# Kernel tuning notes

Measured on AMD Instinct MI355X. Metric: run time of the kernel, lower is better.

Reference implementation:

```python
import jax, jax.numpy as jnp
import numpy as np

HID, NH, HD = 1024, 16, 64
WIN = 512
DFF, NE, TOPK = 4096, 8, 2
B, S = 1, 2048
EPS = 1e-6


def _rope_rotation_matrix(seq_len, head_dim):
    # Block-diagonal 2x2 rotation matrices per position (standard RoPE as a fused matrix).
    pos = np.arange(seq_len, dtype=np.float64)
    inv_freq = 1.0 / (10000.0 ** (np.arange(0, head_dim, 2, dtype=np.float64) / head_dim))
    ang = pos[:, None] * inv_freq[None, :]            # [S, HD/2]
    c, s = np.cos(ang), np.sin(ang)
    R = np.zeros((seq_len, head_dim, head_dim), np.float32)
    i = np.arange(0, head_dim, 2)
    R[:, i, i] = c
    R[:, i + 1, i + 1] = c
    R[:, i, i + 1] = -s
    R[:, i + 1, i] = s
    return jnp.asarray(R)


def setup_inputs() -> dict:
    key = jax.random.key(0)
    ks = jax.random.split(key, 10)
    init = lambda k, shape, scale=0.02: (jax.random.normal(k, shape, jnp.float32) * scale)
    return {
        "x": jax.random.normal(ks[0], (B, S, HID), jnp.float32),
        "rotation_matrix": _rope_rotation_matrix(S, HD),
        "rms1_w": jnp.ones((HID,), jnp.float32),
        "wq": init(ks[1], (HID, HID)),
        "wk": init(ks[2], (HID, HID)),
        "wv": init(ks[3], (HID, HID)),
        "wo": init(ks[4], (HID, HID)),
        "rms2_w": jnp.ones((HID,), jnp.float32),
        "gate_w": init(ks[5], (HID, NE)),
        "w1": init(ks[6], (NE, HID, DFF)),
        "w2": init(ks[7], (NE, DFF, HID)),
        "w3": init(ks[8], (NE, HID, DFF)),
    }


def _rmsnorm(x, w):
    return x * jax.lax.rsqrt(jnp.mean(x * x, axis=-1, keepdims=True) + EPS) * w


def reference(x, rotation_matrix, rms1_w, wq, wk, wv, wo, rms2_w, gate_w, w1, w2, w3):
    b, s, _ = x.shape
    # --- sliding-window attention with fused RoPE rotation matrix ---
    y = _rmsnorm(x, rms1_w)
    q = (y @ wq).reshape(b, s, NH, HD).transpose(0, 2, 1, 3)  # bhsd
    k = (y @ wk).reshape(b, s, NH, HD).transpose(0, 2, 1, 3)
    v = (y @ wv).reshape(b, s, NH, HD).transpose(0, 2, 1, 3)
    q = jnp.einsum('bhsd,sde->bhse', q, rotation_matrix)
    k = jnp.einsum('bhsd,sde->bhse', k, rotation_matrix)
    scores = jnp.einsum('bhqd,bhkd->bhqk', q, k) / np.float32(np.sqrt(HD))
    idx = jnp.arange(s)
    mask = (idx[:, None] >= idx[None, :]) & (idx[:, None] - idx[None, :] < WIN)
    scores = jnp.where(mask[None, None], scores, jnp.float32(-1e9))
    att = jax.nn.softmax(scores, axis=-1)
    attn_out = jnp.einsum('bhqk,bhkd->bhqd', att, v)
    attn_out = attn_out.transpose(0, 2, 1, 3).reshape(b, s, HID) @ wo
    x = x + attn_out
    # --- MoE SwiGLU FFN with top-k routing ---
    y = _rmsnorm(x, rms2_w)
    t = y.reshape(b * s, HID)                                  # [T, D]
    logits = t @ gate_w                                        # [T, E]
    top_v, top_i = jax.lax.top_k(logits, TOPK)
    gates = jax.nn.softmax(top_v, axis=-1)                     # [T, K]
    w_full = jnp.zeros((b * s, NE), t.dtype).at[
        jnp.arange(b * s)[:, None], top_i].set(gates)          # [T, E] sparse routing weights
    h = jax.nn.silu(jnp.einsum('td,edf->etf', t, w1)) * jnp.einsum('td,edf->etf', t, w3)
    expert_out = jnp.einsum('etf,efd->etd', h, w2)             # [E, T, D]
    moe = jnp.einsum('te,etd->td', w_full, expert_out).reshape(b, s, HID)
    return x + moe
```

## Files before the change

### kernel.cpp

```cpp
#include <hip/hip_runtime.h>
#include <hip/hip_bf16.h>
#include <stdint.h>


#define S_ 2048
#define HID_ 1024
#define NH_ 16
#define HD_ 64
#define WIN_ 512
#define DFF_ 4096
#define NE_ 8

typedef unsigned short u16;
typedef __attribute__((ext_vector_type(8))) short short8;
typedef __attribute__((ext_vector_type(4))) float f32x4;

__device__ __forceinline__ u16 f2bf(float f) {
  union { float f; unsigned u; } v; v.f = f;
  unsigned r = (v.u + 0x7FFFu + ((v.u >> 16) & 1u)) >> 16;
  return (u16)r;
}
__device__ __forceinline__ float bf2f(u16 b) {
  union { unsigned u; float f; } v; v.u = ((unsigned)b) << 16;
  return v.f;
}

__device__ __forceinline__ void gload16(const void* g, void* l) {
  __builtin_amdgcn_global_load_lds(
      (const __attribute__((address_space(1))) void*)g,
      (__attribute__((address_space(3))) void*)l, 16, 0, 0);
}

template <int N>
__device__ __forceinline__ void waitcnt_vm() {
  static_assert(N == 0 || N == 4 || N == 8 || N == 12 || N == 16 || N == 24,
                "unsupported vmcnt");
  if constexpr (N == 0) asm volatile("s_waitcnt vmcnt(0)" ::: "memory");
  else if constexpr (N == 4) asm volatile("s_waitcnt vmcnt(4)" ::: "memory");
  else if constexpr (N == 8) asm volatile("s_waitcnt vmcnt(8)" ::: "memory");
  else if constexpr (N == 12) asm volatile("s_waitcnt vmcnt(12)" ::: "memory");
  else if constexpr (N == 16) asm volatile("s_waitcnt vmcnt(16)" ::: "memory");
  else if constexpr (N == 24) asm volatile("s_waitcnt vmcnt(24)" ::: "memory");
}

__global__ __launch_bounds__(256) void convT_f32_k(const float* __restrict__ W,
                                                   u16* __restrict__ WT,
                                                   int K, int N, size_t matStride) {
  __shared__ u16 t[64][72];
  const float* Wm = W + (size_t)blockIdx.z * matStride;
  u16* WTm = WT + (size_t)blockIdx.z * matStride;
  int n0 = blockIdx.x * 64, k0 = blockIdx.y * 64;
  int tid = threadIdx.x;
  int cw = (tid & 15) * 4, rr = tid >> 4;
#pragma unroll
  for (int p = 0; p < 4; ++p) {
    int r = p * 16 + rr;
    float4 v = *(const float4*)&Wm[(size_t)(k0 + r) * N + n0 + cw];
    t[cw][r] = f2bf(v.x);
    t[cw + 1][r] = f2bf(v.y);
    t[cw + 2][r] = f2bf(v.z);
    t[cw + 3][r] = f2bf(v.w);
  }
  __syncthreads();
#pragma unroll
  for (int p = 0; p < 4; ++p) {
    int n = p * 16 + rr;
    ushort4 pk = *(const ushort4*)&t[n][cw];
    *(ushort4*)&WTm[(size_t)(n0 + n) * K + k0 + cw] = pk;
  }
}

__global__ __launch_bounds__(256) void convT_qkvo_k(const float* __restrict__ wq,
                                                    const float* __restrict__ wk,
                                                    const float* __restrict__ wv,
                                                    const float* __restrict__ wo,
                                                    u16* __restrict__ outT) {
  __shared__ u16 t[64][72];
  int z = blockIdx.z;
  const float* Wm = (z == 0) ? wq : (z == 1) ? wk : (z == 2) ? wv : wo;
  u16* WTm = outT + (size_t)z * HID_ * HID_;
  int n0 = blockIdx.x * 64, k0 = blockIdx.y * 64;
  int tid = threadIdx.x;
  int cw = (tid & 15) * 4, rr = tid >> 4;
#pragma unroll
  for (int p = 0; p < 4; ++p) {
    int r = p * 16 + rr;
    float4 v = *(const float4*)&Wm[(size_t)(k0 + r) * HID_ + n0 + cw];
    t[cw][r] = f2bf(v.x);
    t[cw + 1][r] = f2bf(v.y);
    t[cw + 2][r] = f2bf(v.z);
    t[cw + 3][r] = f2bf(v.w);
  }
  __syncthreads();
#pragma unroll
  for (int p = 0; p < 4; ++p) {
    int n = p * 16 + rr;
    ushort4 pk = *(const ushort4*)&t[n][cw];
    *(ushort4*)&WTm[(size_t)(n0 + n) * HID_ + k0 + cw] = pk;
  }
}

__global__ __launch_bounds__(256) void convT_u16_k(const u16* __restrict__ W,
                                                   u16* __restrict__ WT,
                                                   int K, int N, size_t matStride) {
  __shared__ u16 t[64][66];
  const u16* Wm = W + (size_t)blockIdx.z * matStride;
  u16* WTm = WT + (size_t)blockIdx.z * matStride;
  int n0 = blockIdx.x * 64, k0 = blockIdx.y * 64;
  int tid = threadIdx.x;
  int c2 = (tid & 31) * 2, rr = tid >> 5;
#pragma unroll
  for (int it = 0; it < 8; ++it) {
    int r = it * 8 + rr;
    unsigned vv = *(const unsigned*)&Wm[(size_t)(k0 + r) * N + n0 + c2];
    t[c2][r] = (u16)vv;
    t[c2 + 1][r] = (u16)(vv >> 16);
  }
  __syncthreads();
#pragma unroll
  for (int it = 0; it < 8; ++it) {
    int n = it * 8 + rr;
    unsigned pk = (unsigned)t[n][c2] | ((unsigned)t[n][c2 + 1] << 16);
    *(unsigned*)&WTm[(size_t)(n0 + n) * K + k0 + c2] = pk;
  }
}

__global__ __launch_bounds__(256) void rope_tab_k(const float* __restrict__ rot,
                                                  float* __restrict__ cost,
                                                  float* __restrict__ sint) {
  int id = blockIdx.x * 256 + threadIdx.x;
  if (id >= S_ * 32) return;
  int s = id >> 5, j = id & 31;
  cost[id] = rot[(size_t)s * 4096 + (size_t)(2 * j) * 64 + 2 * j];
  sint[id] = rot[(size_t)s * 4096 + (size_t)(2 * j + 1) * 64 + 2 * j];
}

__global__ __launch_bounds__(256) void rms1_k(const float* __restrict__ x,
                                              const float* __restrict__ rw,
                                              u16* __restrict__ y) {
  int row = blockIdx.x, tid = threadIdx.x;
  const float4 v = *(const float4*)&x[(size_t)row * HID_ + tid * 4];
  float ss = v.x * v.x + v.y * v.y + v.z * v.z + v.w * v.w;
#pragma unroll
  for (int o = 32; o; o >>= 1) ss += __shfl_xor(ss, o);
  __shared__ float red[4];
  if ((tid & 63) == 0) red[tid >> 6] = ss;
  __syncthreads();
  float rstd = rsqrtf((red[0] + red[1] + red[2] + red[3]) * (1.f / HID_) + 1e-6f);
  const float4 w4 = *(const float4*)&rw[tid * 4];
  ushort4 o4;
  o4.x = f2bf(v.x * rstd * w4.x);
  o4.y = f2bf(v.y * rstd * w4.y);
  o4.z = f2bf(v.z * rstd * w4.z);
  o4.w = f2bf(v.w * rstd * w4.w);
  *(ushort4*)&y[(size_t)row * HID_ + tid * 4] = o4;
}

__global__ __launch_bounds__(256) void rms2_gate_k(const float* __restrict__ x2,
                                                   const float* __restrict__ rw,
                                                   const float* __restrict__ gw,
                                                   u16* __restrict__ y2,
                                                   float* __restrict__ logits) {
  int row = blockIdx.x, tid = threadIdx.x;
  int wv = tid >> 6, ln = tid & 63;
  const float4 v = *(const float4*)&x2[(size_t)row * HID_ + tid * 4];
  float ss = v.x * v.x + v.y * v.y + v.z * v.z + v.w * v.w;
#pragma unroll
  for (int o = 32; o; o >>= 1) ss += __shfl_xor(ss, o);
  __shared__ float red[4];
  __shared__ float lred[4][8];
  if (ln == 0) red[wv] = ss;
  __syncthreads();
  float rstd = rsqrtf((red[0] + red[1] + red[2] + red[3]) * (1.f / HID_) + 1e-6f);
  const float4 w4 = *(const float4*)&rw[tid * 4];
  float yv[4];
  yv[0] = v.x * rstd * w4.x; yv[1] = v.y * rstd * w4.y;
  yv[2] = v.z * rstd * w4.z; yv[3] = v.w * rstd * w4.w;
  ushort4 o4;
  o4.x = f2bf(yv[0]); o4.y = f2bf(yv[1]); o4.z = f2bf(yv[2]); o4.w = f2bf(yv[3]);
  *(ushort4*)&y2[(size_t)row * HID_ + tid * 4] = o4;
  float le[8] = {0, 0, 0, 0, 0, 0, 0, 0};
  int d0 = tid * 4;
#pragma unroll
  for (int j = 0; j < 4; ++j) {
    const float* grow = &gw[(size_t)(d0 + j) * NE_];
#pragma unroll
    for (int e = 0; e < 8; ++e) le[e] += yv[j] * grow[e];
  }
#pragma unroll
  for (int e = 0; e < 8; ++e) {
    float t = le[e];
#pragma unroll
    for (int o = 32; o; o >>= 1) t += __shfl_xor(t, o);
    le[e] = t;
  }
  if (ln == 0)
#pragma unroll
    for (int e = 0; e < 8; ++e) lred[wv][e] = le[e];
  __syncthreads();
  if (tid < 8)
    logits[(size_t)row * NE_ + tid] =
        lred[0][tid] + lred[1][tid] + lred[2][tid] + lred[3][tid];
}

__global__ __launch_bounds__(1024) void route_k(const float* __restrict__ logits,
                                                int* __restrict__ topi,
                                                float* __restrict__ topg,
                                                int* __restrict__ counts,
                                                int* __restrict__ ebase,
                                                int* __restrict__ slot_token,
                                                int* __restrict__ slot_of) {
  __shared__ int cnt[8], bas[8], rnk[8];
  int tid = threadIdx.x;
  if (tid < 8) { cnt[tid] = 0; rnk[tid] = 0; }
  __syncthreads();
  int e0[2], e1[2];
  float g0[2], g1[2];
#pragma unroll
  for (int s = 0; s < 2; ++s) {
    int t = tid * 2 + s;
    const float* lg = &logits[(size_t)t * NE_];
    float v0 = -1e30f; int i0 = 0;
#pragma unroll
    for (int e = 0; e < 8; ++e) {
      float x = lg[e];
      if (x > v0) { v0 = x; i0 = e; }
    }
    float v1 = -1e30f; int i1 = 0;
#pragma unroll
    for (int e = 0; e < 8; ++e) {
      if (e == i0) continue;
      float x = lg[e];
      if (x > v1) { v1 = x; i1 = e; }
    }
    float ex = __expf(v1 - v0);
    e0[s] = i0; e1[s] = i1;
    g0[s] = 1.f / (1.f + ex);
    g1[s] = ex / (1.f + ex);
    topi[t * 2] = i0; topi[t * 2 + 1] = i1;
    topg[t * 2] = g0[s]; topg[t * 2 + 1] = g1[s];
    atomicAdd(&cnt[i0], 1);
    atomicAdd(&cnt[i1], 1);
  }
  __syncthreads();
  if (tid == 0) {
    int s = 0;
    for (int e = 0; e < 8; ++e) { bas[e] = s; s += cnt[e]; }
  }
  __syncthreads();
#pragma unroll
  for (int s = 0; s < 2; ++s) {
    int t = tid * 2 + s;
    int p0 = bas[e0[s]] + atomicAdd(&rnk[e0[s]], 1);
    int p1 = bas[e1[s]] + atomicAdd(&rnk[e1[s]], 1);
    slot_token[p0] = t; slot_token[p1] = t;
    slot_of[t * 2] = p0; slot_of[t * 2 + 1] = p1;
  }
  if (tid < 8) { counts[tid] = cnt[tid]; ebase[tid] = bas[tid]; }
}

template <int MODE, int SLOTS>
__global__ __launch_bounds__(256, (SLOTS <= 3 ? 3 : (SLOTS <= 5 ? 2 : 1)))
void gemm3_k(
    const u16* __restrict__ A, const u16* __restrict__ B0,
    const u16* __restrict__ B1, const u16* __restrict__ B2, int K,
    const int* __restrict__ ecnt, const int* __restrict__ ebase,
    const float* __restrict__ cost, const float* __restrict__ sint,
    const float* __restrict__ xres, float* __restrict__ outf,
    u16* __restrict__ o0, u16* __restrict__ o1, u16* __restrict__ o2) {
  constexpr int WVM = 4 * (SLOTS - 2);
  __shared__ alignas(16) char smem[SLOTS * 16384];

  int n0 = blockIdx.x * 128, m0 = blockIdx.y * 128;
  int cnt = 0, base = 0, kc = 0;
  const u16* Bp;
  u16* outb = o0;
  float* pout = outf;
  int rope = 0;
  if constexpr (MODE == 0) {
    int z = blockIdx.z;
    Bp = (z == 0) ? B0 : (z == 1) ? B1 : B2;
    outb = (z == 0) ? o0 : (z == 1) ? o1 : o2;
    rope = (z < 2) ? 1 : 0;
  } else if constexpr (MODE == 1) {
    Bp = B0;
  } else if constexpr (MODE == 4) {
    int e = blockIdx.z >> 1;
    kc = blockIdx.z & 1;
    cnt = ecnt[e]; base = ebase[e];
    if (m0 >= cnt) return;
    Bp = B0 + (size_t)e * HID_ * DFF_;
    pout = outf + (size_t)kc * ((size_t)2 * S_ * HID_);
  } else {
    int e = blockIdx.z;
    cnt = ecnt[e]; base = ebase[e];
    if (m0 >= cnt) return;
    Bp = B0 + (size_t)e * HID_ * DFF_;
  }

  int tid = threadIdx.x, w = tid >> 6, l = tid & 63, lo = l & 15, g = l >> 4;
  int wm = w >> 1, wn = w & 1;
  int KT = K >> 5;
  size_t rb = (MODE == 4) ? (size_t)DFF_ * 2 : (size_t)K * 2;
  size_t kcoff = (MODE == 4) ? (size_t)kc * (size_t)(DFF_ / 2) * 2 : 0;

  int lrow = l >> 2, lu = l & 3;
  const char* pA[2];
  const char* pB[2];
  int ldOff[2];
#pragma unroll
  for (int j = 0; j < 2; ++j) {
    int rA = j * 64 + w * 16 + lrow;
    int swz = (lu ^ ((rA >> 1) & 3)) << 4;
    size_t arow;
    if constexpr (MODE == 3 || MODE == 4) {
      arow = (size_t)(base + min(m0 + rA, cnt - 1));
    } else {
      arow = (size_t)(m0 + rA);
    }
    pA[j] = (const char*)A + arow * rb + kcoff + swz;
    pB[j] = (const char*)Bp + (size_t)(n0 + rA) * rb + kcoff + swz;
    ldOff[j] = (j * 64 + w * 16) * 64;
  }

  auto stage = [&](int t) {
    char* s = smem + (t % SLOTS) * 16384;
    size_t kb = (size_t)t * 64;
    gload16(pA[0] + kb, s + ldOff[0]);
    gload16(pA[1] + kb, s + ldOff[1]);
    gload16(pB[0] + kb, s + 8192 + ldOff[0]);
    gload16(pB[1] + kb, s + 8192 + ldOff[1]);
  };

  f32x4 acc[4][4];
#pragma unroll
  for (int i = 0; i < 4; ++i)
#pragma unroll
    for (int j = 0; j < 4; ++j) acc[i][j] = (f32x4){0.f, 0.f, 0.f, 0.f};

#pragma unroll
  for (int s = 0; s < SLOTS - 1; ++s) stage(min(s, KT - 1));
  waitcnt_vm<WVM>();
  __builtin_amdgcn_s_barrier();

  for (int t = 0; t < KT; ++t) {
    char* s = smem + (t % SLOTS) * 16384;
    stage(min(t + SLOTS - 1, KT - 1));
    short8 afr[4], bfr[4];
#pragma unroll
    for (int mi = 0; mi < 4; ++mi) {
      int r = wm * 64 + mi * 16 + lo;
      afr[mi] = *(const short8*)(s + r * 64 + ((g ^ ((r >> 1) & 3)) << 4));
    }
#pragma unroll
    for (int ni = 0; ni < 4; ++ni) {
      int r = wn * 64 + ni * 16 + lo;
      bfr[ni] = *(const short8*)(s + 8192 + r * 64 + ((g ^ ((r >> 1) & 3)) << 4));
    }
    asm volatile("s_waitcnt lgkmcnt(0)" ::: "memory");
    __builtin_amdgcn_s_setprio(1);
#pragma unroll
    for (int mi = 0; mi < 4; ++mi)
#pragma unroll
      for (int ni = 0; ni < 4; ++ni)
        acc[mi][ni] = __builtin_amdgcn_mfma_f32_16x16x32_bf16(afr[mi], bfr[ni], acc[mi][ni], 0, 0, 0);
    __builtin_amdgcn_s_setprio(0);
    if (t + 1 < KT)
      waitcnt_vm<WVM>();
    else
      waitcnt_vm<0>();
    __builtin_amdgcn_s_barrier();
  }
  asm volatile("s_waitcnt vmcnt(0) lgkmcnt(0)" ::: "memory");

#pragma unroll
  for (int mi = 0; mi < 4; ++mi) {
    int lr = wm * 64 + mi * 16 + g * 4;
#pragma unroll
    for (int ni = 0; ni < 4; ++ni) {
      int c = n0 + wn * 64 + ni * 16 + lo;
#pragma unroll
      for (int r = 0; r < 4; ++r) {
        float v = acc[mi][ni][r];
        if constexpr (MODE == 0) {
          int row = m0 + lr + r;
          float p = __shfl_xor(v, 1);
          if (rope) {
            int dd = c & 63;
            float co = cost[(size_t)row * 32 + (dd >> 1)];
            float si = sint[(size_t)row * 32 + (dd >> 1)];
            v = (dd & 1) ? (co * v - si * p) : (co * v + si * p);
          }
          outb[((size_t)(c >> 6) * S_ + row) * HD_ + (c & 63)] = f2bf(v);
        } else if constexpr (MODE == 1) {
          int row = m0 + lr + r;
          outf[(size_t)row * HID_ + c] = v + xres[(size_t)row * HID_ + c];
        } else if constexpr (MODE == 4) {
          int m = m0 + lr + r;
          if (m < cnt) pout[(size_t)(base + m) * HID_ + c] = v;
        } else {
          int m = m0 + lr + r;
          if (m < cnt) outb[(size_t)(base + m) * HID_ + c] = f2bf(v);
        }
      }
    }
  }
}

template <int TPB, int MODE>
__global__ __launch_bounds__(TPB, 2) void gemm5_k(
    const u16* __restrict__ A, const u16* __restrict__ B0,
    const u16* __restrict__ B1, int K, const int* __restrict__ ecnt,
    const int* __restrict__ ebase, const int* __restrict__ slot_token,
    u16* __restrict__ o0, u16* __restrict__ o1) {
  constexpr int NW = TPB / 64;
  constexpr int WN = NW / 2;
  constexpr int BM = TPB / 2;
  constexpr int MROW = BM / 2;
  constexpr int MI = MROW / 16;
  constexpr int MH = MI / 2;
  constexpr int ABYTES = BM * 128;
  __shared__ alignas(16) char smem[ABYTES * 4];
  char* ldsA = smem;
  char* ldsB = smem + 2 * ABYTES;

  int n0 = blockIdx.x * BM, m0 = blockIdx.y * BM;
  int cnt = 0, base = 0;
  const u16* Bp;
  u16* outb;
  {
    int e = blockIdx.z >> 1, mat = blockIdx.z & 1;
    cnt = ecnt[e]; base = ebase[e];
    if (m0 >= cnt) return;
    Bp = (mat ? B1 : B0) + (size_t)e * DFF_ * HID_;
    outb = mat ? o1 : o0;
  }

  int tid = threadIdx.x, w = tid >> 6, l = tid & 63, lo = l & 15, g = l >> 4;
  int wm = w / WN, wn = w % WN;
  int KT = K >> 6;
  size_t rb = (size_t)K * 2;

  int lrow = l >> 3, lu = l & 7;
  const char* pA[4];
  const char* pB[4];
  int ldOff[4];
#pragma unroll
  for (int j = 0; j < 4; ++j) {
    int rA = j * (BM / 4) + w * 8 + lrow;
    int swz = (lu ^ (rA & 7)) << 4;
    size_t arow = (size_t)slot_token[base + min(m0 + rA, cnt - 1)];
    pA[j] = (const char*)A + arow * rb + swz;
    pB[j] = (const char*)Bp + (size_t)(n0 + rA) * rb + swz;
    ldOff[j] = (j * (BM / 4) + w * 8) * 128;
  }

  auto stA = [&](int t, int j) {
    gload16(pA[j] + (size_t)t * 128, ldsA + (t & 1) * ABYTES + ldOff[j]);
  };
  auto stB = [&](int t, int j) {
    gload16(pB[j] + (size_t)t * 128, ldsB + (t & 1) * ABYTES + ldOff[j]);
  };
  auto rdA = [&](int d, int mi, int kh) {
    int row = wm * MROW + mi * 16 + lo;
    return *(const short8*)(ldsA + d * ABYTES + row * 128 +
                            (((kh * 4 + g) ^ (row & 7)) << 4));
  };
  auto rdB = [&](int d, int ni, int kh) {
    int row = wn * 64 + ni * 16 + lo;
    return *(const short8*)(ldsB + d * ABYTES + row * 128 +
                            (((kh * 4 + g) ^ (row & 7)) << 4));
  };

  f32x4 acc[MI][4];
#pragma unroll
  for (int i = 0; i < MI; ++i)
#pragma unroll
    for (int j = 0; j < 4; ++j) acc[i][j] = (f32x4){0.f, 0.f, 0.f, 0.f};

  stB(0, 0); stB(0, 1); stB(0, 2); stB(0, 3);
  stA(0, 0); stA(0, 2);
  stA(0, 1); stA(0, 3);
  {
    int t1 = min(1, KT - 1);
    stA(t1, 0); stA(t1, 2);
  }
  asm volatile("s_waitcnt vmcnt(4)" ::: "memory");
  __builtin_amdgcn_s_barrier();

  for (int t = 0; t < KT; ++t) {
    int d = t & 1;
    int tn = min(t + 1, KT - 1);
    int tn2 = min(t + 2, KT - 1);
    short8 afr[MH], bfr[4];
    stB(tn, 0); stB(tn, 1);
#pragma unroll
    for (int i = 0; i < MH; ++i) afr[i] = rdA(d, i, 0);
#pragma unroll
    for (int n = 0; n < 4; ++n) bfr[n] = rdB(d, n, 0);
    asm volatile("s_waitcnt lgkmcnt(0)" ::: "memory");
    __builtin_amdgcn_s_setprio(1);
#pragma unroll
    for (int i = 0; i < MH; ++i)
#pragma unroll
      for (int n = 0; n < 4; ++n)
        acc[i][n] = __builtin_amdgcn_mfma_f32_16x16x32_bf16(afr[i], bfr[n], acc[i][n], 0, 0, 0);
    __builtin_amdgcn_s_setprio(0);
    asm volatile("s_waitcnt vmcnt(4)" ::: "memory");
    __builtin_amdgcn_s_barrier();
    stB(tn, 2); stB(tn, 3);
#pragma unroll
    for (int i = 0; i < MH; ++i) afr[i] = rdA(d, MH + i, 0);
    asm volatile("s_waitcnt lgkmcnt(0)" ::: "memory");
    __builtin_amdgcn_s_setprio(1);
#pragma unroll
    for (int i = 0; i < MH; ++i)
#pragma unroll
      for (int n = 0; n < 4; ++n)
        acc[MH + i][n] = __builtin_amdgcn_mfma_f32_16x16x32_bf16(afr[i], bfr[n], acc[MH + i][n], 0, 0, 0);
    __builtin_amdgcn_s_setprio(0);
    __builtin_amdgcn_s_barrier();
    stA(tn, 1); stA(tn, 3);
#pragma unroll
    for (int i = 0; i < MH; ++i) afr[i] = rdA(d, i, 1);
#pragma unroll
    for (int n = 0; n < 4; ++n) bfr[n] = rdB(d, n, 1);
    asm volatile("s_waitcnt lgkmcnt(0)" ::: "memory");
    __builtin_amdgcn_s_setprio(1);
#pragma unroll
    for (int i = 0; i < MH; ++i)
#pragma unroll
      for (int n = 0; n < 4; ++n)
        acc[i][n] = __builtin_amdgcn_mfma_f32_16x16x32_bf16(afr[i], bfr[n], acc[i][n], 0, 0, 0);
    __builtin_amdgcn_s_setprio(0);
    __builtin_amdgcn_s_barrier();
    stA(tn2, 0); stA(tn2, 2);
#pragma unroll
    for (int i = 0; i < MH; ++i) afr[i] = rdA(d, MH + i, 1);
    asm volatile("s_waitcnt lgkmcnt(0)" ::: "memory");
    __builtin_amdgcn_s_setprio(1);
#pragma unroll
    for (int i = 0; i < MH; ++i)
#pragma unroll
      for (int n = 0; n < 4; ++n)
        acc[MH + i][n] = __builtin_amdgcn_mfma_f32_16x16x32_bf16(afr[i], bfr[n], acc[MH + i][n], 0, 0, 0);
    __builtin_amdgcn_s_setprio(0);
    asm volatile("s_waitcnt vmcnt(4)" ::: "memory");
    __builtin_amdgcn_s_barrier();
  }
  asm volatile("s_waitcnt vmcnt(0) lgkmcnt(0)" ::: "memory");

#pragma unroll
  for (int mi = 0; mi < MI; ++mi) {
    int lr = wm * MROW + mi * 16 + g * 4;
#pragma unroll
    for (int ni = 0; ni < 4; ++ni) {
      int c = n0 + wn * 64 + ni * 16 + lo;
#pragma unroll
      for (int r = 0; r < 4; ++r) {
        int m = m0 + lr + r;
        if (m < cnt) outb[(size_t)(base + m) * DFF_ + c] = f2bf(acc[mi][ni][r]);
      }
    }
  }
}

__global__ __launch_bounds__(256) void swiglu_k(u16* __restrict__ h1,
                                                const u16* __restrict__ h3) {
  size_t i = ((size_t)blockIdx.x * 256 + threadIdx.x) * 8;
  short8 a = *(const short8*)(h1 + i);
  short8 b = *(const short8*)(h3 + i);
  short8 o;
#pragma unroll
  for (int j = 0; j < 8; ++j) {
    float x = bf2f((u16)a[j]), y = bf2f((u16)b[j]);
    float s = x / (1.f + __expf(-x));
    o[j] = (short)f2bf(s * y);
  }
  *(short8*)(h1 + i) = o;
}

__global__ __launch_bounds__(256) void attn_k(const u16* __restrict__ qh,
                                              const u16* __restrict__ kh,
                                              const u16* __restrict__ vht,
                                              u16* __restrict__ attn) {
  int qt = blockIdx.x, h = blockIdx.y;
  int tid = threadIdx.x, w = tid >> 6, l = tid & 63, lo = l & 15, g = l >> 4;
  __shared__ alignas(16) char Ks[8192];
  __shared__ alignas(16) char Vs[8192];
  __shared__ alignas(16) char Ps[8192];
  char* Pw = Ps + w * 2048;
  int q0 = qt * 64, qw = q0 + w * 16;
  const u16* qhh = qh + ((size_t)h * S_ + qw) * HD_;
  short8 bq0 = *(const short8*)(qhh + lo * 64 + g * 8);
  short8 bq1 = *(const short8*)(qhh + lo * 64 + 32 + g * 8);
  int q = qw + lo;
  float m_run = -1e30f, l_run = 0.f;
  f32x4 o[4];
#pragma unroll
  for (int i = 0; i < 4; ++i) o[i] = (f32x4){0.f, 0.f, 0.f, 0.f};
  int kt0 = max(0, q0 - (WIN_ - 1)) >> 6;
  for (int kt = kt0; kt <= qt; ++kt) {
    int kb = kt * 64;
    {
      int r0 = w * 16 + (l >> 3), r1 = r0 + 8;
      int uu = l & 7;
      short8 k0v = *(const short8*)(kh + ((size_t)h * S_ + kb + r0) * HD_ + uu * 8);
      short8 k1v = *(const short8*)(kh + ((size_t)h * S_ + kb + r1) * HD_ + uu * 8);
      short8 v0v = *(const short8*)(vht + ((size_t)h * HD_ + r0) * S_ + kb + uu * 8);
      short8 v1v = *(const short8*)(vht + ((size_t)h * HD_ + r1) * S_ + kb + uu * 8);
      *(short8*)(Ks + r0 * 128 + ((uu ^ (r0 & 7)) << 4)) = k0v;
      *(short8*)(Ks + r1 * 128 + ((uu ^ (r1 & 7)) << 4)) = k1v;
      *(short8*)(Vs + r0 * 128 + ((uu ^ (r0 & 7)) << 4)) = v0v;
      *(short8*)(Vs + r1 * 128 + ((uu ^ (r1 & 7)) << 4)) = v1v;
    }
    __syncthreads();
    f32x4 st[4];
#pragma unroll
    for (int kf = 0; kf < 4; ++kf) {
      int key = kf * 16 + lo;
      short8 a0 = *(const short8*)(Ks + key * 128 + ((g ^ (key & 7)) << 4));
      short8 a1 = *(const short8*)(Ks + key * 128 + (((4 + g) ^ (key & 7)) << 4));
      f32x4 z = (f32x4){0.f, 0.f, 0.f, 0.f};
      z = __builtin_amdgcn_mfma_f32_16x16x32_bf16(a0, bq0, z, 0, 0, 0);
      z = __builtin_amdgcn_mfma_f32_16x16x32_bf16(a1, bq1, z, 0, 0, 0);
      st[kf] = z;
    }
    float p[16];
    float tmax = -1e30f;
#pragma unroll
    for (int kf = 0; kf < 4; ++kf)
#pragma unroll
      for (int r = 0; r < 4; ++r) {
        int key = kb + kf * 16 + g * 4 + r;
        float s = st[kf][r] * 0.125f;
        bool okm = (key <= q) && (q - key < WIN_);
        s = okm ? s : -1e30f;
        p[kf * 4 + r] = s;
        tmax = fmaxf(tmax, s);
      }
    tmax = fmaxf(tmax, __shfl_xor(tmax, 16));
    tmax = fmaxf(tmax, __shfl_xor(tmax, 32));
    float m_new = fmaxf(m_run, tmax);
    float corr = __expf(m_run - m_new);
    float tsum = 0.f;
#pragma unroll
    for (int i = 0; i < 16; ++i) {
      float pe = (p[i] > -1e29f) ? __expf(p[i] - m_new) : 0.f;
      p[i] = pe;
      tsum += pe;
    }
    tsum += __shfl_xor(tsum, 16);
    tsum += __shfl_xor(tsum, 32);
    l_run = l_run * corr + tsum;
    m_run = m_new;
#pragma unroll
    for (int kf = 0; kf < 4; ++kf)
#pragma unroll
      for (int pr = 0; pr < 2; ++pr) {
        int keyloc = kf * 16 + g * 4 + pr * 2;
        unsigned pk = (unsigned)f2bf(p[kf * 4 + pr * 2]) |
                      ((unsigned)f2bf(p[kf * 4 + pr * 2 + 1]) << 16);
        *(unsigned*)(Pw + lo * 128 + (((keyloc >> 3) ^ (lo & 7)) << 4) +
                     (keyloc & 7) * 2) = pk;
      }
    float c0 = __shfl(corr, g * 4 + 0), c1 = __shfl(corr, g * 4 + 1);
    float c2 = __shfl(corr, g * 4 + 2), c3 = __shfl(corr, g * 4 + 3);
#pragma unroll
    for (int nf = 0; nf < 4; ++nf) {
      o[nf][0] *= c0; o[nf][1] *= c1; o[nf][2] *= c2; o[nf][3] *= c3;
    }
    short8 ap0 = *(const short8*)(Pw + lo * 128 + ((g ^ (lo & 7)) << 4));
    short8 ap1 = *(const short8*)(Pw + lo * 128 + (((4 + g) ^ (lo & 7)) << 4));
#pragma unroll
    for (int nf = 0; nf < 4; ++nf) {
      int d = nf * 16 + lo;
      short8 v0 = *(const short8*)(Vs + d * 128 + ((g ^ (d & 7)) << 4));
      short8 v1 = *(const short8*)(Vs + d * 128 + (((4 + g) ^ (d & 7)) << 4));
      o[nf] = __builtin_amdgcn_mfma_f32_16x16x32_bf16(ap0, v0, o[nf], 0, 0, 0);
      o[nf] = __builtin_amdgcn_mfma_f32_16x16x32_bf16(ap1, v1, o[nf], 0, 0, 0);
    }
    __syncthreads();
  }
  float linv = 1.f / l_run;
  float i0 = __shfl(linv, g * 4 + 0), i1 = __shfl(linv, g * 4 + 1);
  float i2 = __shfl(linv, g * 4 + 2), i3 = __shfl(linv, g * 4 + 3);
#pragma unroll
  for (int nf = 0; nf < 4; ++nf) {
    int d = nf * 16 + lo;
    attn[(size_t)(qw + g * 4 + 0) * HID_ + h * HD_ + d] = f2bf(o[nf][0] * i0);
    attn[(size_t)(qw + g * 4 + 1) * HID_ + h * HD_ + d] = f2bf(o[nf][1] * i1);
    attn[(size_t)(qw + g * 4 + 2) * HID_ + h * HD_ + d] = f2bf(o[nf][2] * i2);
    attn[(size_t)(qw + g * 4 + 3) * HID_ + h * HD_ + d] = f2bf(o[nf][3] * i3);
  }
}

__global__ __launch_bounds__(256) void combine_k(float* __restrict__ out,
                                                 const float* __restrict__ part,
                                                 const int* __restrict__ slot_of,
                                                 const float* __restrict__ topg) {
  int row = blockIdx.x, tid = threadIdx.x;
  int d0 = tid * 4;
  const size_t PS = (size_t)2 * S_ * HID_;
  int p0 = slot_of[row * 2], p1 = slot_of[row * 2 + 1];
  float g0 = topg[row * 2], g1 = topg[row * 2 + 1];
  float4 cur = *(float4*)&out[(size_t)row * HID_ + d0];
  float4 a0 = *(const float4*)&part[(size_t)p0 * HID_ + d0];
  float4 a1 = *(const float4*)&part[PS + (size_t)p0 * HID_ + d0];
  float4 b0 = *(const float4*)&part[(size_t)p1 * HID_ + d0];
  float4 b1 = *(const float4*)&part[PS + (size_t)p1 * HID_ + d0];
  cur.x += g0 * (a0.x + a1.x) + g1 * (b0.x + b1.x);
  cur.y += g0 * (a0.y + a1.y) + g1 * (b0.y + b1.y);
  cur.z += g0 * (a0.z + a1.z) + g1 * (b0.z + b1.z);
  cur.w += g0 * (a0.w + a1.w) + g1 * (b0.w + b1.w);
  *(float4*)&out[(size_t)row * HID_ + d0] = cur;
}

extern "C" void kernel_launch(void* const* d_in, const int* in_sizes, int n_in,
                              void* d_out, int out_size, void* d_ws,
                              size_t ws_size, hipStream_t stream) {
  const float* x = (const float*)d_in[0];
  const float* rot = (const float*)d_in[1];
  const float* r1w = (const float*)d_in[2];
  const float* wq = (const float*)d_in[3];
  const float* wk = (const float*)d_in[4];
  const float* wv = (const float*)d_in[5];
  const float* wo = (const float*)d_in[6];
  const float* r2w = (const float*)d_in[7];
  const float* gw = (const float*)d_in[8];
  const float* w1 = (const float*)d_in[9];
  const float* w2 = (const float*)d_in[10];
  const float* w3 = (const float*)d_in[11];
  float* out = (float*)d_out;

  char* ws = (char*)d_ws;
  size_t off = 0;
  auto alloc = [&](size_t bytes) {
    char* p = ws + off;
    off += (bytes + 255) & ~(size_t)255;
    return p;
  };
  const size_t MB4 = (size_t)S_ * HID_ * 2;
  u16* wqkvoT = (u16*)alloc((size_t)4 * HID_ * HID_ * 2);
  u16* wqT = wqkvoT;
  u16* wkT = wqkvoT + (size_t)HID_ * HID_;
  u16* wvT = wqkvoT + (size_t)2 * HID_ * HID_;
  u16* woT = wqkvoT + (size_t)3 * HID_ * HID_;
  u16* w1T = (u16*)alloc((size_t)NE_ * DFF_ * HID_ * 2);
  u16* w3T = (u16*)alloc((size_t)NE_ * DFF_ * HID_ * 2);
  u16* w2T = (u16*)alloc((size_t)NE_ * HID_ * DFF_ * 2);
  char* uni = alloc((size_t)2 * S_ * DFF_ * 2);
  u16* ybf = (u16*)(uni);
  u16* qh = (u16*)(uni + MB4);
  u16* kh = (u16*)(uni + 2 * MB4);
  u16* vh = (u16*)(uni + 3 * MB4);
  u16* vht = (u16*)(uni + 4 * MB4);
  u16* attnb = (u16*)(uni + 5 * MB4);
  u16* h3 = (u16*)uni;
  float* partials = (float*)uni;
  u16* y2bf = (u16*)alloc(MB4);
  u16* h1 = (u16*)alloc((size_t)2 * S_ * DFF_ * 2);
  float* cost = (float*)alloc((size_t)S_ * 32 * 4);
  float* sint = (float*)alloc((size_t)S_ * 32 * 4);
  float* logits = (float*)alloc((size_t)S_ * NE_ * 4);
  int* topi = (int*)alloc((size_t)S_ * 2 * 4);
  float* topg = (float*)alloc((size_t)S_ * 2 * 4);
  int* ints = (int*)alloc(256);
  int* counts = ints;
  int* ebase = ints + 8;
  int* slot_token = (int*)alloc((size_t)2 * S_ * 4);
  int* slot_of = (int*)alloc((size_t)S_ * 2 * 4);
  (void)ws_size; (void)in_sizes; (void)n_in; (void)out_size;

  convT_qkvo_k<<<dim3(16, 16, 4), 256, 0, stream>>>(wq, wk, wv, wo, wqkvoT);
  convT_f32_k<<<dim3(64, 16, 8), 256, 0, stream>>>(w1, w1T, HID_, DFF_, (size_t)HID_ * DFF_);
  convT_f32_k<<<dim3(64, 16, 8), 256, 0, stream>>>(w3, w3T, HID_, DFF_, (size_t)HID_ * DFF_);
  convT_f32_k<<<dim3(16, 64, 8), 256, 0, stream>>>(w2, w2T, DFF_, HID_, (size_t)DFF_ * HID_);

  rope_tab_k<<<dim3(256), 256, 0, stream>>>(rot, cost, sint);
  rms1_k<<<dim3(S_), 256, 0, stream>>>(x, r1w, ybf);

  gemm3_k<0, 5><<<dim3(8, 16, 3), 256, 0, stream>>>(
      ybf, wqT, wkT, wvT, HID_, nullptr, nullptr, cost, sint, nullptr,
      nullptr, qh, kh, vh);
  convT_u16_k<<<dim3(1, 32, 16), 256, 0, stream>>>(vh, vht, S_, HD_, (size_t)S_ * HD_);

  attn_k<<<dim3(32, 16), 256, 0, stream>>>(qh, kh, vht, attnb);

  gemm3_k<1, 5><<<dim3(8, 16, 1), 256, 0, stream>>>(
      attnb, woT, nullptr, nullptr, HID_, nullptr, nullptr, nullptr, nullptr,
      x, out, nullptr, nullptr, nullptr);

  rms2_gate_k<<<dim3(S_), 256, 0, stream>>>(out, r2w, gw, y2bf, logits);
  route_k<<<dim3(1), 1024, 0, stream>>>(logits, topi, topg, counts, ebase,
                                        slot_token, slot_of);

  gemm5_k<512, 2><<<dim3(16, 8, 16), 512, 0, stream>>>(
      y2bf, w1T, w3T, HID_, counts, ebase, slot_token, h1, h3);
  swiglu_k<<<dim3(8192), 256, 0, stream>>>(h1, h3);
  gemm3_k<4, 4><<<dim3(8, 16, 16), 256, 0, stream>>>(
      h1, w2T, nullptr, nullptr, DFF_ / 2, counts, ebase, nullptr, nullptr,
      nullptr, partials, nullptr, nullptr, nullptr);
  combine_k<<<dim3(S_), 256, 0, stream>>>(out, partials, slot_of, topg);
}
```

Before: 417.7 us.

## Restructure MoE up-projection GEMM pipeline to two phases and merge w1/w3 conversion

The gemm5 main loop drops from four sub-phases per K tile to two. Each phase now loads both k-halves of the fragments at once, and all A and B loads for the next tile are issued together, with no prefetch two tiles ahead. This halves the barriers per iteration but holds more fragment registers and gives less load/compute overlap. The separate w1 and w3 weight transpose/convert launches are also merged into one launch over a contiguous buffer, removing one kernel launch.

```diff
diff --git a/kernel.cpp b/kernel.cpp
--- a/kernel.cpp
+++ b/kernel.cpp
@@ -33,22 +33,28 @@
 
 template <int N>
 __device__ __forceinline__ void waitcnt_vm() {
-  static_assert(N == 0 || N == 4 || N == 8 || N == 12 || N == 16 || N == 24,
-                "unsupported vmcnt");
+  static_assert(N == 0 || N == 2 || N == 4 || N == 6 || N == 8 || N == 12 ||
+                N == 16 || N == 24, "unsupported vmcnt");
   if constexpr (N == 0) asm volatile("s_waitcnt vmcnt(0)" ::: "memory");
+  else if constexpr (N == 2) asm volatile("s_waitcnt vmcnt(2)" ::: "memory");
   else if constexpr (N == 4) asm volatile("s_waitcnt vmcnt(4)" ::: "memory");
+  else if constexpr (N == 6) asm volatile("s_waitcnt vmcnt(6)" ::: "memory");
   else if constexpr (N == 8) asm volatile("s_waitcnt vmcnt(8)" ::: "memory");
   else if constexpr (N == 12) asm volatile("s_waitcnt vmcnt(12)" ::: "memory");
   else if constexpr (N == 16) asm volatile("s_waitcnt vmcnt(16)" ::: "memory");
   else if constexpr (N == 24) asm volatile("s_waitcnt vmcnt(24)" ::: "memory");
 }
 
-__global__ __launch_bounds__(256) void convT_f32_k(const float* __restrict__ W,
+__global__ __launch_bounds__(256) void convT_f32_k(const float* __restrict__ Wa,
+                                                   const float* __restrict__ Wb,
+                                                   int zsplit,
                                                    u16* __restrict__ WT,
                                                    int K, int N, size_t matStride) {
   __shared__ u16 t[64][72];
-  const float* Wm = W + (size_t)blockIdx.z * matStride;
-  u16* WTm = WT + (size_t)blockIdx.z * matStride;
+  int z = blockIdx.z;
+  const float* Wm = (z < zsplit ? Wa + (size_t)z * matStride
+                                : Wb + (size_t)(z - zsplit) * matStride);
+  u16* WTm = WT + (size_t)z * matStride;
   int n0 = blockIdx.x * 64, k0 = blockIdx.y * 64;
   int tid = threadIdx.x;
   int cw = (tid & 15) * 4, rr = tid >> 4;
@@ -407,37 +413,29 @@
   }
 }
 
-template <int TPB, int MODE>
-__global__ __launch_bounds__(TPB, 2) void gemm5_k(
+__global__ __launch_bounds__(512, 2) void gemm5_k(
     const u16* __restrict__ A, const u16* __restrict__ B0,
     const u16* __restrict__ B1, int K, const int* __restrict__ ecnt,
     const int* __restrict__ ebase, const int* __restrict__ slot_token,
     u16* __restrict__ o0, u16* __restrict__ o1) {
-  constexpr int NW = TPB / 64;
-  constexpr int WN = NW / 2;
-  constexpr int BM = TPB / 2;
-  constexpr int MROW = BM / 2;
-  constexpr int MI = MROW / 16;
-  constexpr int MH = MI / 2;
+  constexpr int BM = 256;
+  constexpr int MROW = 128;
+  constexpr int MI = 8;
+  constexpr int MH = 4;
   constexpr int ABYTES = BM * 128;
   __shared__ alignas(16) char smem[ABYTES * 4];
   char* ldsA = smem;
   char* ldsB = smem + 2 * ABYTES;
 
   int n0 = blockIdx.x * BM, m0 = blockIdx.y * BM;
-  int cnt = 0, base = 0;
-  const u16* Bp;
-  u16* outb;
-  {
-    int e = blockIdx.z >> 1, mat = blockIdx.z & 1;
-    cnt = ecnt[e]; base = ebase[e];
-    if (m0 >= cnt) return;
-    Bp = (mat ? B1 : B0) + (size_t)e * DFF_ * HID_;
-    outb = mat ? o1 : o0;
-  }
+  int e = blockIdx.z >> 1, mat = blockIdx.z & 1;
+  int cnt = ecnt[e], base = ebase[e];
+  if (m0 >= cnt) return;
+  const u16* Bp = (mat ? B1 : B0) + (size_t)e * DFF_ * HID_;
+  u16* outb = mat ? o1 : o0;
 
   int tid = threadIdx.x, w = tid >> 6, l = tid & 63, lo = l & 15, g = l >> 4;
-  int wm = w / WN, wn = w % WN;
+  int wm = w >> 2, wn = w & 3;
   int KT = K >> 6;
   size_t rb = (size_t)K * 2;
 
@@ -447,12 +445,12 @@
   int ldOff[4];
 #pragma unroll
   for (int j = 0; j < 4; ++j) {
-    int rA = j * (BM / 4) + w * 8 + lrow;
+    int rA = j * 64 + w * 8 + lrow;
     int swz = (lu ^ (rA & 7)) << 4;
     size_t arow = (size_t)slot_token[base + min(m0 + rA, cnt - 1)];
     pA[j] = (const char*)A + arow * rb + swz;
     pB[j] = (const char*)Bp + (size_t)(n0 + rA) * rb + swz;
-    ldOff[j] = (j * (BM / 4) + w * 8) * 128;
+    ldOff[j] = (j * 64 + w * 8) * 128;
   }
 
   auto stA = [&](int t, int j) {
@@ -479,73 +477,56 @@
     for (int j = 0; j < 4; ++j) acc[i][j] = (f32x4){0.f, 0.f, 0.f, 0.f};
 
   stB(0, 0); stB(0, 1); stB(0, 2); stB(0, 3);
-  stA(0, 0); stA(0, 2);
-  stA(0, 1); stA(0, 3);
-  {
-    int t1 = min(1, KT - 1);
-    stA(t1, 0); stA(t1, 2);
-  }
-  asm volatile("s_waitcnt vmcnt(4)" ::: "memory");
+  stA(0, 0); stA(0, 2); stA(0, 1); stA(0, 3);
+  waitcnt_vm<2>();
   __builtin_amdgcn_s_barrier();
 
   for (int t = 0; t < KT; ++t) {
     int d = t & 1;
     int tn = min(t + 1, KT - 1);
-    int tn2 = min(t + 2, KT - 1);
-    short8 afr[MH], bfr[4];
-    stB(tn, 0); stB(tn, 1);
-#pragma unroll
-    for (int i = 0; i < MH; ++i) afr[i] = rdA(d, i, 0);
-#pragma unroll
-    for (int n = 0; n < 4; ++n) bfr[n] = rdB(d, n, 0);
+    short8 afr[MH][2], bfr[4][2];
+    stB(tn, 0); stB(tn, 1); stB(tn, 2); stB(tn, 3);
+#pragma unroll
+    for (int i = 0; i < MH; ++i) {
+      afr[i][0] = rdA(d, i, 0);
+      afr[i][1] = rdA(d, i, 1);
+    }
+#pragma unroll
+    for (int n = 0; n < 4; ++n) {
+      bfr[n][0] = rdB(d, n, 0);
+      bfr[n][1] = rdB(d, n, 1);
+    }
     asm volatile("s_waitcnt lgkmcnt(0)" ::: "memory");
     __builtin_amdgcn_s_setprio(1);
 #pragma unroll
-    for (int i = 0; i < MH; ++i)
-#pragma unroll
-      for (int n = 0; n < 4; ++n)
-        acc[i][n] = __builtin_amdgcn_mfma_f32_16x16x32_bf16(afr[i], bfr[n], acc[i][n], 0, 0, 0);
+    for (int kh = 0; kh < 2; ++kh)
+#pragma unroll
+      for (int i = 0; i < MH; ++i)
+#pragma unroll
+        for (int n = 0; n < 4; ++n)
+          acc[i][n] = __builtin_amdgcn_mfma_f32_16x16x32_bf16(
+              afr[i][kh], bfr[n][kh], acc[i][n], 0, 0, 0);
     __builtin_amdgcn_s_setprio(0);
-    asm volatile("s_waitcnt vmcnt(4)" ::: "memory");
+    waitcnt_vm<4>();
     __builtin_amdgcn_s_barrier();
-    stB(tn, 2); stB(tn, 3);
-#pragma unroll
-    for (int i = 0; i < MH; ++i) afr[i] = rdA(d, MH + i, 0);
+    stA(tn, 0); stA(tn, 2); stA(tn, 1); stA(tn, 3);
+#pragma unroll
+    for (int i = 0; i < MH; ++i) {
+      afr[i][0] = rdA(d, MH + i, 0);
+      afr[i][1] = rdA(d, MH + i, 1);
+    }
     asm volatile("s_waitcnt lgkmcnt(0)" ::: "memory");
     __builtin_amdgcn_s_setprio(1);
 #pragma unroll
-    for (int i = 0; i < MH; ++i)
-#pragma unroll
-      for (int n = 0; n < 4; ++n)
-        acc[MH + i][n] = __builtin_amdgcn_mfma_f32_16x16x32_bf16(afr[i], bfr[n], acc[MH + i][n], 0, 0, 0);
+    for (int kh = 0; kh < 2; ++kh)
+#pragma unroll
+      for (int i = 0; i < MH; ++i)
+#pragma unroll
+        for (int n = 0; n < 4; ++n)
+          acc[MH + i][n] = __builtin_amdgcn_mfma_f32_16x16x32_bf16(
+              afr[i][kh], bfr[n][kh], acc[MH + i][n], 0, 0, 0);
     __builtin_amdgcn_s_setprio(0);
-    __builtin_amdgcn_s_barrier();
-    stA(tn, 1); stA(tn, 3);
-#pragma unroll
-    for (int i = 0; i < MH; ++i) afr[i] = rdA(d, i, 1);
-#pragma unroll
-    for (int n = 0; n < 4; ++n) bfr[n] = rdB(d, n, 1);
-    asm volatile("s_waitcnt lgkmcnt(0)" ::: "memory");
-    __builtin_amdgcn_s_setprio(1);
-#pragma unroll
-    for (int i = 0; i < MH; ++i)
-#pragma unroll
-      for (int n = 0; n < 4; ++n)
-        acc[i][n] = __builtin_amdgcn_mfma_f32_16x16x32_bf16(afr[i], bfr[n], acc[i][n], 0, 0, 0);
-    __builtin_amdgcn_s_setprio(0);
-    __builtin_amdgcn_s_barrier();
-    stA(tn2, 0); stA(tn2, 2);
-#pragma unroll
-    for (int i = 0; i < MH; ++i) afr[i] = rdA(d, MH + i, 1);
-    asm volatile("s_waitcnt lgkmcnt(0)" ::: "memory");
-    __builtin_amdgcn_s_setprio(1);
-#pragma unroll
-    for (int i = 0; i < MH; ++i)
-#pragma unroll
-      for (int n = 0; n < 4; ++n)
-        acc[MH + i][n] = __builtin_amdgcn_mfma_f32_16x16x32_bf16(afr[i], bfr[n], acc[MH + i][n], 0, 0, 0);
-    __builtin_amdgcn_s_setprio(0);
-    asm volatile("s_waitcnt vmcnt(4)" ::: "memory");
+    waitcnt_vm<2>();
     __builtin_amdgcn_s_barrier();
   }
   asm volatile("s_waitcnt vmcnt(0) lgkmcnt(0)" ::: "memory");
@@ -746,8 +727,9 @@
   u16* wkT = wqkvoT + (size_t)HID_ * HID_;
   u16* wvT = wqkvoT + (size_t)2 * HID_ * HID_;
   u16* woT = wqkvoT + (size_t)3 * HID_ * HID_;
-  u16* w1T = (u16*)alloc((size_t)NE_ * DFF_ * HID_ * 2);
-  u16* w3T = (u16*)alloc((size_t)NE_ * DFF_ * HID_ * 2);
+  u16* w13T = (u16*)alloc((size_t)2 * NE_ * DFF_ * HID_ * 2);
+  u16* w1T = w13T;
+  u16* w3T = w13T + (size_t)NE_ * DFF_ * HID_;
   u16* w2T = (u16*)alloc((size_t)NE_ * HID_ * DFF_ * 2);
   char* uni = alloc((size_t)2 * S_ * DFF_ * 2);
   u16* ybf = (u16*)(uni);
@@ -773,9 +755,10 @@
   (void)ws_size; (void)in_sizes; (void)n_in; (void)out_size;
 
   convT_qkvo_k<<<dim3(16, 16, 4), 256, 0, stream>>>(wq, wk, wv, wo, wqkvoT);
-  convT_f32_k<<<dim3(64, 16, 8), 256, 0, stream>>>(w1, w1T, HID_, DFF_, (size_t)HID_ * DFF_);
-  convT_f32_k<<<dim3(64, 16, 8), 256, 0, stream>>>(w3, w3T, HID_, DFF_, (size_t)HID_ * DFF_);
-  convT_f32_k<<<dim3(16, 64, 8), 256, 0, stream>>>(w2, w2T, DFF_, HID_, (size_t)DFF_ * HID_);
+  convT_f32_k<<<dim3(64, 16, 16), 256, 0, stream>>>(w1, w3, 8, w13T, HID_, DFF_,
+                                                    (size_t)HID_ * DFF_);
+  convT_f32_k<<<dim3(16, 64, 8), 256, 0, stream>>>(w2, nullptr, 8, w2T, DFF_,
+                                                   HID_, (size_t)DFF_ * HID_);
 
   rope_tab_k<<<dim3(256), 256, 0, stream>>>(rot, cost, sint);
   rms1_k<<<dim3(S_), 256, 0, stream>>>(x, r1w, ybf);
@@ -795,7 +778,7 @@
   route_k<<<dim3(1), 1024, 0, stream>>>(logits, topi, topg, counts, ebase,
                                         slot_token, slot_of);
 
-  gemm5_k<512, 2><<<dim3(16, 8, 16), 512, 0, stream>>>(
+  gemm5_k<<<dim3(16, 8, 16), 512, 0, stream>>>(
       y2bf, w1T, w3T, HID_, counts, ebase, slot_token, h1, h3);
   swiglu_k<<<dim3(8192), 256, 0, stream>>>(h1, h3);
   gemm3_k<4, 4><<<dim3(8, 16, 16), 256, 0, stream>>>(
```

Result: no change. 416.7 us (-0.2%).
